# Performance work log

Measured on AMD Instinct MI355X. Metric: run time of the kernel, lower is better.

The kernel has to match this reference:

```python
import jax, jax.numpy as jnp
import numpy as np


def setup_inputs() -> dict:
    key = jax.random.key(0)
    k1, k2, k3, k4, k5 = jax.random.split(key, 5)
    B, T, K, H, A = 16, 256, 256, 512, 49
    return {
        "hiddens_des": jax.random.normal(k1, (B, K, H), dtype=jnp.float32),
        "hiddens_title": jax.random.normal(k2, (B, T, H), dtype=jnp.float32),
        "Wv": jax.random.normal(k3, (A, H), dtype=jnp.float32) * (1.0 / np.sqrt(H)),
        "Wg": jax.random.normal(k4, (A, H), dtype=jnp.float32) * (1.0 / np.sqrt(H)),
        "Wh": jax.random.normal(k5, (1, A), dtype=jnp.float32) * (1.0 / np.sqrt(A)),
    }


def reference(hiddens_des, hiddens_title, Wv, Wg, Wh):
    # Dropout is identity (eval mode) for the deterministic baseline.
    # content_v: (B,1,K,49) + (B,T,1,49) -> (B,T,K,49)
    cv = jnp.einsum("bkh,ah->bka", hiddens_des, Wv)    # (B,K,49)
    cg = jnp.einsum("bth,ah->bta", hiddens_title, Wg)  # (B,T,49)
    content = cv[:, None, :, :] + cg[:, :, None, :]     # (B,T,K,49)
    z = jnp.einsum("btka,a->btk", jnp.tanh(content), Wh[0])  # (B,T,K)
    alpha = jax.nn.softmax(z, axis=-1)                  # softmax over K
    c_hat = jnp.einsum("btk,bkh->bth", alpha, hiddens_des)  # (B,T,H)
    return (c_hat, alpha)
```

## Files before the change

### kernel.cpp

```cpp
#include <hip/hip_runtime.h>
#include <hip/hip_bf16.h>

#define B_ 16
#define T_ 256
#define K_ 256
#define H_ 512
#define A_ 49
#define APAD 64

typedef __attribute__((ext_vector_type(8))) short short8;
typedef __attribute__((ext_vector_type(4))) float f32x4;

__device__ __forceinline__ ushort f2bf(float f) {
    uint u = __builtin_bit_cast(uint, f);
    u += 0x7FFF + ((u >> 16) & 1);
    return (ushort)(u >> 16);
}

__device__ __forceinline__ void cvt_hilo(float4 v0, float4 v1, short8& hi, short8& lo) {
    float v[8] = {v0.x, v0.y, v0.z, v0.w, v1.x, v1.y, v1.z, v1.w};
    #pragma unroll
    for (int i = 0; i < 8; ++i) {
        ushort h = f2bf(v[i]);
        float hf = __builtin_bit_cast(float, (uint)h << 16);
        hi[i] = (short)h;
        lo[i] = (short)f2bf(v[i] - hf);
    }
}

__device__ __forceinline__ float sig2(float x) {
    float e = __expf(2.f * x);
    return __builtin_amdgcn_rcpf(e + 1.f);
}

__global__ __launch_bounds__(256) void kW(const float* __restrict__ Wv,
                                          const float* __restrict__ Wg,
                                          ushort* __restrict__ Whl)
{
    int blk = blockIdx.x;
    int m = blk >> 6, row = blk & 63;
    const float* W = m ? Wg : Wv;
    int tid = threadIdx.x;
    ushort* hi = Whl + ((size_t)(m * 2 + 0) * 64 + row) * H_;
    ushort* lo = Whl + ((size_t)(m * 2 + 1) * 64 + row) * H_;
    #pragma unroll
    for (int c = tid; c < H_; c += 256) {
        float v = (row < A_) ? W[(size_t)row * H_ + c] : 0.f;
        ushort h = f2bf(v);
        float hf = __builtin_bit_cast(float, (uint)h << 16);
        hi[c] = h;
        lo[c] = f2bf(v - hf);
    }
}

__global__ __launch_bounds__(256) void kAP(const float* __restrict__ des,
                                           const float* __restrict__ title,
                                           const ushort* __restrict__ Whl,
                                           float* __restrict__ cvT,
                                           float* __restrict__ cg,
                                           ushort* __restrict__ desT)
{
    __shared__ float Tls[32][33];
    int tid = threadIdx.x;

    if (blockIdx.x >= 512) {
        int tb = blockIdx.x - 512;
        int b = tb >> 7, rem = tb & 127;
        int k0 = (rem >> 4) * 32, h0 = (rem & 15) * 32;
        int kk = tid >> 3, c4 = (tid & 7) * 4;
        float4 v = *(const float4*)(des + ((size_t)(b * K_ + k0 + kk) * H_) + h0 + c4);
        Tls[kk][c4 + 0] = v.x; Tls[kk][c4 + 1] = v.y;
        Tls[kk][c4 + 2] = v.z; Tls[kk][c4 + 3] = v.w;
        __syncthreads();
        int hh = tid >> 3;
        ushort4 o;
        o.x = f2bf(Tls[c4 + 0][hh]);
        o.y = f2bf(Tls[c4 + 1][hh]);
        o.z = f2bf(Tls[c4 + 2][hh]);
        o.w = f2bf(Tls[c4 + 3][hh]);
        *(ushort4*)(desT + ((size_t)(b * H_ + h0 + hh) * K_) + k0 + c4) = o;
        return;
    }

    int wv = tid >> 6, lane = tid & 63;
    int tile = blockIdx.x;
    bool isDes = tile < 256;
    int lr = lane & 15, lc = lane >> 4;
    int g = wv;

    const float* X = isDes ? (des + (size_t)tile * 16 * H_)
                           : (title + (size_t)(tile - 256) * 16 * H_);
    int m = isDes ? 0 : 1;
    const ushort* whiP = Whl + ((size_t)(m * 2 + 0) * 64 + g * 16 + lr) * H_ + lc * 8;
    const ushort* wloP = Whl + ((size_t)(m * 2 + 1) * 64 + g * 16 + lr) * H_ + lc * 8;
    const float*  xp0  = X + (size_t)lr * H_ + lc * 8;

    f32x4 acc = {};

    for (int k0 = 0; k0 < H_; k0 += 32) {
        float4 xv0 = *(const float4*)(xp0 + k0);
        float4 xv1 = *(const float4*)(xp0 + k0 + 4);
        short8 xhi, xlo;
        cvt_hilo(xv0, xv1, xhi, xlo);
        short8 whi = *(const short8*)(whiP + k0);
        short8 wlo = *(const short8*)(wloP + k0);
        if (isDes) {
            acc = __builtin_amdgcn_mfma_f32_16x16x32_bf16(whi, xhi, acc, 0, 0, 0);
            acc = __builtin_amdgcn_mfma_f32_16x16x32_bf16(whi, xlo, acc, 0, 0, 0);
            acc = __builtin_amdgcn_mfma_f32_16x16x32_bf16(wlo, xhi, acc, 0, 0, 0);
        } else {
            acc = __builtin_amdgcn_mfma_f32_16x16x32_bf16(xhi, whi, acc, 0, 0, 0);
            acc = __builtin_amdgcn_mfma_f32_16x16x32_bf16(xlo, whi, acc, 0, 0, 0);
            acc = __builtin_amdgcn_mfma_f32_16x16x32_bf16(xhi, wlo, acc, 0, 0, 0);
        }
    }

    if (isDes) {
        int krows = tile * 16;
        int b = krows >> 8, kb = krows & 255;
        #pragma unroll
        for (int r = 0; r < 4; ++r) {
            int a = g * 16 + lc * 4 + r;
            cvT[((size_t)b * APAD + a) * K_ + kb + lr] = acc[r];
        }
    } else {
        int trows = (tile - 256) * 16;
        #pragma unroll
        for (int r = 0; r < 4; ++r) {
            int row = trows + lc * 4 + r;
            cg[(size_t)row * APAD + g * 16 + lr] = acc[r];
        }
    }
}

__global__ __launch_bounds__(512) void kZ(const float* __restrict__ cvT,
                                          const float* __restrict__ cg,
                                          const float* __restrict__ Wh,
                                          const ushort* __restrict__ desT,
                                          float* __restrict__ alpha,
                                          float* __restrict__ chat)
{
    __shared__ float  sCg[8][APAD];
    __shared__ float  sWh[APAD];
    __shared__ float  sRedM[8][4];
    __shared__ float  sRedS[8][4];
    __shared__ ushort sA[16][K_ + 8];

    int bid = blockIdx.x;
    int b  = bid & 15;
    int t0 = (bid >> 4) * 8;
    int tid = threadIdx.x;
    int k  = tid & 255;
    int tg = tid >> 8;
    int tb = tg * 4;

    if (tid < 128) {
        int row = tid >> 4, c = (tid & 15) * 4;
        *(float4*)(&sCg[row][c]) =
            *(const float4*)(cg + (size_t)(b * T_ + t0 + row) * APAD + c);
    } else if (tid < 128 + APAD) {
        int a = tid - 128;
        sWh[a] = (a < A_) ? Wh[a] : 0.f;
    }
    {
        uint* zp = (uint*)&sA[8][0];
        #pragma unroll
        for (int i = tid; i < 1056; i += 512) zp[i] = 0;
    }
    __syncthreads();

    const float* cvp = cvT + (size_t)b * APAD * K_ + k;
    float zacc[4] = {0.f, 0.f, 0.f, 0.f};

    for (int c6 = 0; c6 < 6; ++c6) {
        int a0 = c6 * 8;
        float xa[8];
        #pragma unroll
        for (int i = 0; i < 8; ++i) xa[i] = cvp[(size_t)(a0 + i) * K_];
        float4 w0 = *(const float4*)&sWh[a0];
        float4 w1 = *(const float4*)&sWh[a0 + 4];
        #pragma unroll
        for (int j = 0; j < 4; ++j) {
            float4 c0 = *(const float4*)&sCg[tb + j][a0];
            float4 c1 = *(const float4*)&sCg[tb + j][a0 + 4];
            zacc[j] += w0.x * sig2(xa[0] + c0.x) + w0.y * sig2(xa[1] + c0.y)
                     + w0.z * sig2(xa[2] + c0.z) + w0.w * sig2(xa[3] + c0.w)
                     + w1.x * sig2(xa[4] + c1.x) + w1.y * sig2(xa[5] + c1.y)
                     + w1.z * sig2(xa[6] + c1.z) + w1.w * sig2(xa[7] + c1.w);
        }
    }
    {
        float xa48 = cvp[(size_t)48 * K_];
        float wh = sWh[48];
        #pragma unroll
        for (int j = 0; j < 4; ++j)
            zacc[j] += wh * sig2(xa48 + sCg[tb + j][48]);
    }
    float sw = 0.f;
    #pragma unroll
    for (int q = 0; q < 16; ++q) {
        float4 w4 = *(const float4*)&sWh[q * 4];
        sw += w4.x + w4.y + w4.z + w4.w;
    }
    float z[4];
    #pragma unroll
    for (int j = 0; j < 4; ++j) z[j] = sw - 2.f * zacc[j];

    int wv = tid >> 6, lane = tid & 63, w3 = wv & 3;
    #pragma unroll
    for (int j = 0; j < 4; ++j) {
        float m = z[j];
        #pragma unroll
        for (int off = 32; off > 0; off >>= 1) m = fmaxf(m, __shfl_xor(m, off));
        if (lane == 0) sRedM[tb + j][w3] = m;
    }
    __syncthreads();
    #pragma unroll
    for (int j = 0; j < 4; ++j) {
        int t = tb + j;
        float m = fmaxf(fmaxf(sRedM[t][0], sRedM[t][1]),
                        fmaxf(sRedM[t][2], sRedM[t][3]));
        z[j] = __expf(z[j] - m);
    }
    #pragma unroll
    for (int j = 0; j < 4; ++j) {
        float s = z[j];
        #pragma unroll
        for (int off = 32; off > 0; off >>= 1) s += __shfl_xor(s, off);
        if (lane == 0) sRedS[tb + j][w3] = s;
    }
    __syncthreads();
    #pragma unroll
    for (int j = 0; j < 4; ++j) {
        int t = tb + j;
        float s = sRedS[t][0] + sRedS[t][1] + sRedS[t][2] + sRedS[t][3];
        float rs = __builtin_amdgcn_rcpf(s);
        rs = rs * (2.f - s * rs);
        float al = z[j] * rs;
        alpha[(size_t)(b * T_ + t0 + t) * K_ + k] = al;
        sA[t][k] = f2bf(al);
    }
    __syncthreads();

    int lr = lane & 15, lc = lane >> 4;
    int h0 = wv * 64;
    const ushort* Bp = desT + ((size_t)(b * H_ + h0 + lr)) * K_ + lc * 8;

    short8 af[8];
    #pragma unroll
    for (int s = 0; s < 8; ++s)
        af[s] = *(const short8*)(&sA[lr][s * 32 + lc * 8]);

    f32x4 acc[4] = {};
    #pragma unroll
    for (int j = 0; j < 4; ++j) {
        const ushort* Bj = Bp + (size_t)(j * 16) * K_;
        short8 bf[8];
        #pragma unroll
        for (int s = 0; s < 8; ++s)
            bf[s] = *(const short8*)(Bj + s * 32);
        #pragma unroll
        for (int s = 0; s < 8; ++s)
            acc[j] = __builtin_amdgcn_mfma_f32_16x16x32_bf16(af[s], bf[s], acc[j], 0, 0, 0);
    }

    #pragma unroll
    for (int j = 0; j < 4; ++j) {
        #pragma unroll
        for (int r = 0; r < 4; ++r) {
            int row = lc * 4 + r;
            if (row < 8)
                chat[((size_t)(b * T_ + t0 + row)) * H_ + h0 + j * 16 + lr] = acc[j][r];
        }
    }
}

extern "C" void kernel_launch(void* const* d_in, const int* in_sizes, int n_in,
                              void* d_out, int out_size, void* d_ws, size_t ws_size,
                              hipStream_t stream) {
    const float* des   = (const float*)d_in[0];
    const float* title = (const float*)d_in[1];
    const float* Wv    = (const float*)d_in[2];
    const float* Wg    = (const float*)d_in[3];
    const float* Wh    = (const float*)d_in[4];

    float* chat  = (float*)d_out;
    float* alpha = (float*)d_out + (size_t)B_ * T_ * H_;

    char* ws = (char*)d_ws;
    float*  cvT  = (float*)ws;
    float*  cg   = cvT + (size_t)B_ * APAD * K_;
    ushort* desT = (ushort*)(cg + (size_t)B_ * T_ * APAD);
    ushort* Whl  = desT + (size_t)B_ * H_ * K_;

    hipLaunchKernelGGL(kW, dim3(128), dim3(256), 0, stream, Wv, Wg, Whl);
    hipLaunchKernelGGL(kAP, dim3(2560), dim3(256), 0, stream,
                       des, title, Whl, cvT, cg, desT);
    hipLaunchKernelGGL(kZ, dim3(2 * B_ * (T_ / 16)), dim3(512), 0, stream,
                       cvT, cg, Wh, desT, alpha, chat);
}
```

Before: 56.86 us.

## Fuse projection and attention kernels with a grid-wide atomic barrier

Merges the weight-split kernel into the transpose kernel. Also merges the projection GEMM and the softmax/attention kernel into one persistent 512-block kernel that uses a global atomic counter as a grid barrier between phases. Input rows are staged once into LDS as bf16 hi/lo and shared across waves instead of each wave converting from global memory. This removes one launch and inter-kernel gaps, but it adds a memset, an atomic spin barrier that relies on all 512 blocks being co-resident, and idle waves during the projection phase.

```diff
diff --git a/kernel.cpp b/kernel.cpp
--- a/kernel.cpp
+++ b/kernel.cpp
@@ -7,6 +7,8 @@
 #define H_ 512
 #define A_ 49
 #define APAD 64
+#define GRID2 512
+#define XPAD 520
 
 typedef __attribute__((ext_vector_type(8))) short short8;
 typedef __attribute__((ext_vector_type(4))) float f32x4;
@@ -33,137 +35,158 @@
     return __builtin_amdgcn_rcpf(e + 1.f);
 }
 
-__global__ __launch_bounds__(256) void kW(const float* __restrict__ Wv,
-                                          const float* __restrict__ Wg,
-                                          ushort* __restrict__ Whl)
-{
-    int blk = blockIdx.x;
-    int m = blk >> 6, row = blk & 63;
-    const float* W = m ? Wg : Wv;
-    int tid = threadIdx.x;
-    ushort* hi = Whl + ((size_t)(m * 2 + 0) * 64 + row) * H_;
-    ushort* lo = Whl + ((size_t)(m * 2 + 1) * 64 + row) * H_;
-    #pragma unroll
-    for (int c = tid; c < H_; c += 256) {
-        float v = (row < A_) ? W[(size_t)row * H_ + c] : 0.f;
-        ushort h = f2bf(v);
-        float hf = __builtin_bit_cast(float, (uint)h << 16);
-        hi[c] = h;
-        lo[c] = f2bf(v - hf);
-    }
-}
-
-__global__ __launch_bounds__(256) void kAP(const float* __restrict__ des,
-                                           const float* __restrict__ title,
-                                           const ushort* __restrict__ Whl,
-                                           float* __restrict__ cvT,
-                                           float* __restrict__ cg,
-                                           ushort* __restrict__ desT)
+__global__ __launch_bounds__(256) void kPre(const float* __restrict__ des,
+                                            const float* __restrict__ Wv,
+                                            const float* __restrict__ Wg,
+                                            ushort* __restrict__ Whl,
+                                            ushort* __restrict__ desT)
 {
     __shared__ float Tls[32][33];
     int tid = threadIdx.x;
 
-    if (blockIdx.x >= 512) {
-        int tb = blockIdx.x - 512;
-        int b = tb >> 7, rem = tb & 127;
-        int k0 = (rem >> 4) * 32, h0 = (rem & 15) * 32;
-        int kk = tid >> 3, c4 = (tid & 7) * 4;
-        float4 v = *(const float4*)(des + ((size_t)(b * K_ + k0 + kk) * H_) + h0 + c4);
-        Tls[kk][c4 + 0] = v.x; Tls[kk][c4 + 1] = v.y;
-        Tls[kk][c4 + 2] = v.z; Tls[kk][c4 + 3] = v.w;
-        __syncthreads();
-        int hh = tid >> 3;
-        ushort4 o;
-        o.x = f2bf(Tls[c4 + 0][hh]);
-        o.y = f2bf(Tls[c4 + 1][hh]);
-        o.z = f2bf(Tls[c4 + 2][hh]);
-        o.w = f2bf(Tls[c4 + 3][hh]);
-        *(ushort4*)(desT + ((size_t)(b * H_ + h0 + hh) * K_) + k0 + c4) = o;
+    if (blockIdx.x < 128) {
+        int blk = blockIdx.x;
+        int m = blk >> 6, row = blk & 63;
+        const float* W = m ? Wg : Wv;
+        ushort* hi = Whl + ((size_t)(m * 2 + 0) * 64 + row) * H_;
+        ushort* lo = Whl + ((size_t)(m * 2 + 1) * 64 + row) * H_;
+        #pragma unroll
+        for (int c = tid; c < H_; c += 256) {
+            float v = (row < A_) ? W[(size_t)row * H_ + c] : 0.f;
+            ushort h = f2bf(v);
+            float hf = __builtin_bit_cast(float, (uint)h << 16);
+            hi[c] = h;
+            lo[c] = f2bf(v - hf);
+        }
         return;
     }
 
+    int tb = blockIdx.x - 128;
+    int b = tb >> 7, rem = tb & 127;
+    int k0 = (rem >> 4) * 32, h0 = (rem & 15) * 32;
+    int kk = tid >> 3, c4 = (tid & 7) * 4;
+    float4 v = *(const float4*)(des + ((size_t)(b * K_ + k0 + kk) * H_) + h0 + c4);
+    Tls[kk][c4 + 0] = v.x; Tls[kk][c4 + 1] = v.y;
+    Tls[kk][c4 + 2] = v.z; Tls[kk][c4 + 3] = v.w;
+    __syncthreads();
+    int hh = tid >> 3;
+    ushort4 o;
+    o.x = f2bf(Tls[c4 + 0][hh]);
+    o.y = f2bf(Tls[c4 + 1][hh]);
+    o.z = f2bf(Tls[c4 + 2][hh]);
+    o.w = f2bf(Tls[c4 + 3][hh]);
+    *(ushort4*)(desT + ((size_t)(b * H_ + h0 + hh) * K_) + k0 + c4) = o;
+}
+
+union U2 {
+    struct { ushort xhi[16][XPAD]; ushort xlo[16][XPAD]; } p;
+    struct { float cg[8][APAD]; float wh[APAD];
+             float rm[8][4]; float rs[8][4]; ushort a[16][K_ + 8]; } z;
+};
+
+__global__ __launch_bounds__(512, 4) void kMain(const float* __restrict__ des,
+                                                const float* __restrict__ title,
+                                                const ushort* __restrict__ Whl,
+                                                const float* __restrict__ Wh,
+                                                const ushort* __restrict__ desT,
+                                                float* __restrict__ cvT,
+                                                float* __restrict__ cg,
+                                                float* __restrict__ alpha,
+                                                float* __restrict__ chat,
+                                                uint* __restrict__ counter)
+{
+    __shared__ U2 u;
+    int tid = threadIdx.x;
+    int bid = blockIdx.x;
+    int b = bid & 15;
+    int j = bid >> 4;
+    bool isDes = j < 16;
+
+    const float* Xbase = isDes ? (des + ((size_t)(b * K_ + j * 16)) * H_)
+                               : (title + ((size_t)(b * T_ + (j - 16) * 16)) * H_);
+    {
+        #pragma unroll
+        for (int it = 0; it < 2; ++it) {
+            int eidx = it * 4096 + tid * 8;
+            int r = eidx >> 9, c = eidx & 511;
+            const float* p = Xbase + (size_t)r * H_ + c;
+            float4 v0 = *(const float4*)(p);
+            float4 v1 = *(const float4*)(p + 4);
+            short8 hi, lo;
+            cvt_hilo(v0, v1, hi, lo);
+            *(short8*)&u.p.xhi[r][c] = hi;
+            *(short8*)&u.p.xlo[r][c] = lo;
+        }
+    }
+    __syncthreads();
+
     int wv = tid >> 6, lane = tid & 63;
-    int tile = blockIdx.x;
-    bool isDes = tile < 256;
     int lr = lane & 15, lc = lane >> 4;
-    int g = wv;
-
-    const float* X = isDes ? (des + (size_t)tile * 16 * H_)
-                           : (title + (size_t)(tile - 256) * 16 * H_);
-    int m = isDes ? 0 : 1;
-    const ushort* whiP = Whl + ((size_t)(m * 2 + 0) * 64 + g * 16 + lr) * H_ + lc * 8;
-    const ushort* wloP = Whl + ((size_t)(m * 2 + 1) * 64 + g * 16 + lr) * H_ + lc * 8;
-    const float*  xp0  = X + (size_t)lr * H_ + lc * 8;
-
-    f32x4 acc = {};
-
-    for (int k0 = 0; k0 < H_; k0 += 32) {
-        float4 xv0 = *(const float4*)(xp0 + k0);
-        float4 xv1 = *(const float4*)(xp0 + k0 + 4);
-        short8 xhi, xlo;
-        cvt_hilo(xv0, xv1, xhi, xlo);
-        short8 whi = *(const short8*)(whiP + k0);
-        short8 wlo = *(const short8*)(wloP + k0);
+
+    if (wv < 4) {
+        int g = wv;
+        int m = isDes ? 0 : 1;
+        const ushort* whiP = Whl + ((size_t)(m * 2 + 0) * 64 + g * 16 + lr) * H_ + lc * 8;
+        const ushort* wloP = Whl + ((size_t)(m * 2 + 1) * 64 + g * 16 + lr) * H_ + lc * 8;
+
+        f32x4 acc = {};
+        #pragma unroll 4
+        for (int k0 = 0; k0 < H_; k0 += 32) {
+            short8 whi = *(const short8*)(whiP + k0);
+            short8 wlo = *(const short8*)(wloP + k0);
+            short8 xhi = *(const short8*)&u.p.xhi[lr][k0 + lc * 8];
+            short8 xlo = *(const short8*)&u.p.xlo[lr][k0 + lc * 8];
+            if (isDes) {
+                acc = __builtin_amdgcn_mfma_f32_16x16x32_bf16(whi, xhi, acc, 0, 0, 0);
+                acc = __builtin_amdgcn_mfma_f32_16x16x32_bf16(whi, xlo, acc, 0, 0, 0);
+                acc = __builtin_amdgcn_mfma_f32_16x16x32_bf16(wlo, xhi, acc, 0, 0, 0);
+            } else {
+                acc = __builtin_amdgcn_mfma_f32_16x16x32_bf16(xhi, whi, acc, 0, 0, 0);
+                acc = __builtin_amdgcn_mfma_f32_16x16x32_bf16(xlo, whi, acc, 0, 0, 0);
+                acc = __builtin_amdgcn_mfma_f32_16x16x32_bf16(xhi, wlo, acc, 0, 0, 0);
+            }
+        }
+
         if (isDes) {
-            acc = __builtin_amdgcn_mfma_f32_16x16x32_bf16(whi, xhi, acc, 0, 0, 0);
-            acc = __builtin_amdgcn_mfma_f32_16x16x32_bf16(whi, xlo, acc, 0, 0, 0);
-            acc = __builtin_amdgcn_mfma_f32_16x16x32_bf16(wlo, xhi, acc, 0, 0, 0);
+            int kb = j * 16;
+            #pragma unroll
+            for (int r = 0; r < 4; ++r) {
+                int a = g * 16 + lc * 4 + r;
+                cvT[((size_t)b * APAD + a) * K_ + kb + lr] = acc[r];
+            }
         } else {
-            acc = __builtin_amdgcn_mfma_f32_16x16x32_bf16(xhi, whi, acc, 0, 0, 0);
-            acc = __builtin_amdgcn_mfma_f32_16x16x32_bf16(xlo, whi, acc, 0, 0, 0);
-            acc = __builtin_amdgcn_mfma_f32_16x16x32_bf16(xhi, wlo, acc, 0, 0, 0);
-        }
-    }
-
-    if (isDes) {
-        int krows = tile * 16;
-        int b = krows >> 8, kb = krows & 255;
-        #pragma unroll
-        for (int r = 0; r < 4; ++r) {
-            int a = g * 16 + lc * 4 + r;
-            cvT[((size_t)b * APAD + a) * K_ + kb + lr] = acc[r];
-        }
-    } else {
-        int trows = (tile - 256) * 16;
-        #pragma unroll
-        for (int r = 0; r < 4; ++r) {
-            int row = trows + lc * 4 + r;
-            cg[(size_t)row * APAD + g * 16 + lr] = acc[r];
-        }
-    }
-}
-
-__global__ __launch_bounds__(512) void kZ(const float* __restrict__ cvT,
-                                          const float* __restrict__ cg,
-                                          const float* __restrict__ Wh,
-                                          const ushort* __restrict__ desT,
-                                          float* __restrict__ alpha,
-                                          float* __restrict__ chat)
-{
-    __shared__ float  sCg[8][APAD];
-    __shared__ float  sWh[APAD];
-    __shared__ float  sRedM[8][4];
-    __shared__ float  sRedS[8][4];
-    __shared__ ushort sA[16][K_ + 8];
-
-    int bid = blockIdx.x;
-    int b  = bid & 15;
-    int t0 = (bid >> 4) * 8;
-    int tid = threadIdx.x;
+            int trows = b * T_ + (j - 16) * 16;
+            #pragma unroll
+            for (int r = 0; r < 4; ++r) {
+                int row = trows + lc * 4 + r;
+                cg[(size_t)row * APAD + g * 16 + lr] = acc[r];
+            }
+        }
+    }
+
+    __syncthreads();
+    if (tid == 0) {
+        __hip_atomic_fetch_add(counter, 1u, __ATOMIC_ACQ_REL, __HIP_MEMORY_SCOPE_AGENT);
+        while (__hip_atomic_load(counter, __ATOMIC_ACQUIRE, __HIP_MEMORY_SCOPE_AGENT) < GRID2)
+            __builtin_amdgcn_s_sleep(8);
+    }
+    __syncthreads();
+
+    int t0 = j * 8;
     int k  = tid & 255;
     int tg = tid >> 8;
-    int tb = tg * 4;
+    int tb2 = tg * 4;
 
     if (tid < 128) {
         int row = tid >> 4, c = (tid & 15) * 4;
-        *(float4*)(&sCg[row][c]) =
+        *(float4*)(&u.z.cg[row][c]) =
             *(const float4*)(cg + (size_t)(b * T_ + t0 + row) * APAD + c);
     } else if (tid < 128 + APAD) {
         int a = tid - 128;
-        sWh[a] = (a < A_) ? Wh[a] : 0.f;
+        u.z.wh[a] = (a < A_) ? Wh[a] : 0.f;
     }
     {
-        uint* zp = (uint*)&sA[8][0];
+        uint* zp = (uint*)&u.z.a[8][0];
         #pragma unroll
         for (int i = tid; i < 1056; i += 512) zp[i] = 0;
     }
@@ -177,100 +200,99 @@
         float xa[8];
         #pragma unroll
         for (int i = 0; i < 8; ++i) xa[i] = cvp[(size_t)(a0 + i) * K_];
-        float4 w0 = *(const float4*)&sWh[a0];
-        float4 w1 = *(const float4*)&sWh[a0 + 4];
-        #pragma unroll
-        for (int j = 0; j < 4; ++j) {
-            float4 c0 = *(const float4*)&sCg[tb + j][a0];
-            float4 c1 = *(const float4*)&sCg[tb + j][a0 + 4];
-            zacc[j] += w0.x * sig2(xa[0] + c0.x) + w0.y * sig2(xa[1] + c0.y)
-                     + w0.z * sig2(xa[2] + c0.z) + w0.w * sig2(xa[3] + c0.w)
-                     + w1.x * sig2(xa[4] + c1.x) + w1.y * sig2(xa[5] + c1.y)
-                     + w1.z * sig2(xa[6] + c1.z) + w1.w * sig2(xa[7] + c1.w);
+        float4 w0 = *(const float4*)&u.z.wh[a0];
+        float4 w1 = *(const float4*)&u.z.wh[a0 + 4];
+        #pragma unroll
+        for (int jj = 0; jj < 4; ++jj) {
+            float4 c0 = *(const float4*)&u.z.cg[tb2 + jj][a0];
+            float4 c1 = *(const float4*)&u.z.cg[tb2 + jj][a0 + 4];
+            zacc[jj] += w0.x * sig2(xa[0] + c0.x) + w0.y * sig2(xa[1] + c0.y)
+                      + w0.z * sig2(xa[2] + c0.z) + w0.w * sig2(xa[3] + c0.w)
+                      + w1.x * sig2(xa[4] + c1.x) + w1.y * sig2(xa[5] + c1.y)
+                      + w1.z * sig2(xa[6] + c1.z) + w1.w * sig2(xa[7] + c1.w);
         }
     }
     {
         float xa48 = cvp[(size_t)48 * K_];
-        float wh = sWh[48];
-        #pragma unroll
-        for (int j = 0; j < 4; ++j)
-            zacc[j] += wh * sig2(xa48 + sCg[tb + j][48]);
+        float wh = u.z.wh[48];
+        #pragma unroll
+        for (int jj = 0; jj < 4; ++jj)
+            zacc[jj] += wh * sig2(xa48 + u.z.cg[tb2 + jj][48]);
     }
     float sw = 0.f;
     #pragma unroll
     for (int q = 0; q < 16; ++q) {
-        float4 w4 = *(const float4*)&sWh[q * 4];
+        float4 w4 = *(const float4*)&u.z.wh[q * 4];
         sw += w4.x + w4.y + w4.z + w4.w;
     }
     float z[4];
     #pragma unroll
-    for (int j = 0; j < 4; ++j) z[j] = sw - 2.f * zacc[j];
-
-    int wv = tid >> 6, lane = tid & 63, w3 = wv & 3;
-    #pragma unroll
-    for (int j = 0; j < 4; ++j) {
-        float m = z[j];
-        #pragma unroll
-        for (int off = 32; off > 0; off >>= 1) m = fmaxf(m, __shfl_xor(m, off));
-        if (lane == 0) sRedM[tb + j][w3] = m;
-    }
-    __syncthreads();
-    #pragma unroll
-    for (int j = 0; j < 4; ++j) {
-        int t = tb + j;
-        float m = fmaxf(fmaxf(sRedM[t][0], sRedM[t][1]),
-                        fmaxf(sRedM[t][2], sRedM[t][3]));
-        z[j] = __expf(z[j] - m);
-    }
-    #pragma unroll
-    for (int j = 0; j < 4; ++j) {
-        float s = z[j];
+    for (int jj = 0; jj < 4; ++jj) z[jj] = sw - 2.f * zacc[jj];
+
+    int w3 = wv & 3;
+    #pragma unroll
+    for (int jj = 0; jj < 4; ++jj) {
+        float mx = z[jj];
+        #pragma unroll
+        for (int off = 32; off > 0; off >>= 1) mx = fmaxf(mx, __shfl_xor(mx, off));
+        if (lane == 0) u.z.rm[tb2 + jj][w3] = mx;
+    }
+    __syncthreads();
+    #pragma unroll
+    for (int jj = 0; jj < 4; ++jj) {
+        int t = tb2 + jj;
+        float mx = fmaxf(fmaxf(u.z.rm[t][0], u.z.rm[t][1]),
+                         fmaxf(u.z.rm[t][2], u.z.rm[t][3]));
+        z[jj] = __expf(z[jj] - mx);
+    }
+    #pragma unroll
+    for (int jj = 0; jj < 4; ++jj) {
+        float s = z[jj];
         #pragma unroll
         for (int off = 32; off > 0; off >>= 1) s += __shfl_xor(s, off);
-        if (lane == 0) sRedS[tb + j][w3] = s;
-    }
-    __syncthreads();
-    #pragma unroll
-    for (int j = 0; j < 4; ++j) {
-        int t = tb + j;
-        float s = sRedS[t][0] + sRedS[t][1] + sRedS[t][2] + sRedS[t][3];
+        if (lane == 0) u.z.rs[tb2 + jj][w3] = s;
+    }
+    __syncthreads();
+    #pragma unroll
+    for (int jj = 0; jj < 4; ++jj) {
+        int t = tb2 + jj;
+        float s = u.z.rs[t][0] + u.z.rs[t][1] + u.z.rs[t][2] + u.z.rs[t][3];
         float rs = __builtin_amdgcn_rcpf(s);
         rs = rs * (2.f - s * rs);
-        float al = z[j] * rs;
+        float al = z[jj] * rs;
         alpha[(size_t)(b * T_ + t0 + t) * K_ + k] = al;
-        sA[t][k] = f2bf(al);
-    }
-    __syncthreads();
-
-    int lr = lane & 15, lc = lane >> 4;
+        u.z.a[t][k] = f2bf(al);
+    }
+    __syncthreads();
+
     int h0 = wv * 64;
     const ushort* Bp = desT + ((size_t)(b * H_ + h0 + lr)) * K_ + lc * 8;
 
     short8 af[8];
     #pragma unroll
     for (int s = 0; s < 8; ++s)
-        af[s] = *(const short8*)(&sA[lr][s * 32 + lc * 8]);
+        af[s] = *(const short8*)(&u.z.a[lr][s * 32 + lc * 8]);
 
     f32x4 acc[4] = {};
     #pragma unroll
-    for (int j = 0; j < 4; ++j) {
-        const ushort* Bj = Bp + (size_t)(j * 16) * K_;
+    for (int jj = 0; jj < 4; ++jj) {
+        const ushort* Bj = Bp + (size_t)(jj * 16) * K_;
         short8 bf[8];
         #pragma unroll
         for (int s = 0; s < 8; ++s)
             bf[s] = *(const short8*)(Bj + s * 32);
         #pragma unroll
         for (int s = 0; s < 8; ++s)
-            acc[j] = __builtin_amdgcn_mfma_f32_16x16x32_bf16(af[s], bf[s], acc[j], 0, 0, 0);
-    }
-
-    #pragma unroll
-    for (int j = 0; j < 4; ++j) {
+            acc[jj] = __builtin_amdgcn_mfma_f32_16x16x32_bf16(af[s], bf[s], acc[jj], 0, 0, 0);
+    }
+
+    #pragma unroll
+    for (int jj = 0; jj < 4; ++jj) {
         #pragma unroll
         for (int r = 0; r < 4; ++r) {
             int row = lc * 4 + r;
             if (row < 8)
-                chat[((size_t)(b * T_ + t0 + row)) * H_ + h0 + j * 16 + lr] = acc[j][r];
+                chat[((size_t)(b * T_ + t0 + row)) * H_ + h0 + jj * 16 + lr] = acc[jj][r];
         }
     }
 }
@@ -292,10 +314,11 @@
     float*  cg   = cvT + (size_t)B_ * APAD * K_;
     ushort* desT = (ushort*)(cg + (size_t)B_ * T_ * APAD);
     ushort* Whl  = desT + (size_t)B_ * H_ * K_;
-
-    hipLaunchKernelGGL(kW, dim3(128), dim3(256), 0, stream, Wv, Wg, Whl);
-    hipLaunchKernelGGL(kAP, dim3(2560), dim3(256), 0, stream,
-                       des, title, Whl, cvT, cg, desT);
-    hipLaunchKernelGGL(kZ, dim3(2 * B_ * (T_ / 16)), dim3(512), 0, stream,
-                       cvT, cg, Wh, desT, alpha, chat);
-}
+    uint* counter = (uint*)(Whl + (size_t)4 * 64 * H_);
+
+    hipMemsetAsync(counter, 0, 128, stream);
+    hipLaunchKernelGGL(kPre, dim3(2176), dim3(256), 0, stream,
+                       des, Wv, Wg, Whl, desT);
+    hipLaunchKernelGGL(kMain, dim3(GRID2), dim3(512), 0, stream,
+                       des, title, Whl, Wh, desT, cvT, cg, alpha, chat, counter);
+}
```

Measured after the change: 96.54 us. +69.8%, slower.
